# Kernel optimization log

Hardware: AMD Instinct MI355X
Metric: run time of the kernel (lower is better)

The kernel has to match this reference:

```python
import jax, jax.numpy as jnp
import numpy as np

HID, FFN, NE, TOPK = 1024, 4096, 8, 2


def setup_inputs() -> dict:
    key = jax.random.key(0)
    ks = jax.random.split(key, 4)
    x = jax.random.normal(ks[0], (2, 2048, HID), dtype=jnp.float32)
    # router: nn.Linear(hidden, num_experts, bias=False), init std=0.02; stored as [H, E]
    Wr = jax.random.normal(ks[1], (HID, NE), dtype=jnp.float32) * 0.02
    # per-expert FFN weights stacked on leading expert axis
    W1 = jax.random.normal(ks[2], (NE, HID, FFN), dtype=jnp.float32) * (1.0 / np.sqrt(HID))
    b1 = jnp.zeros((NE, FFN), dtype=jnp.float32)
    W2 = jax.random.normal(ks[3], (NE, FFN, HID), dtype=jnp.float32) * (1.0 / np.sqrt(FFN))
    b2 = jnp.zeros((NE, HID), dtype=jnp.float32)
    return {"x": x, "Wr": Wr, "W1": W1, "b1": b1, "W2": W2, "b2": b2}


def reference(x, Wr, W1, b1, W2, b2):
    B, S, H = x.shape
    E = Wr.shape[1]
    T = B * S
    xf = x.reshape(T, H)                                  # [T, H]
    logits = xf @ Wr                                      # [T, E]
    probs = jax.nn.softmax(logits, axis=-1)
    topk_p, topk_i = jax.lax.top_k(probs, TOPK)           # [T, K]
    topk_p = topk_p / jnp.sum(topk_p, axis=-1, keepdims=True)
    # dense combine weights: c[t, e] = normalized prob if expert e selected for token t else 0
    c = jnp.zeros((T, E), dtype=xf.dtype).at[jnp.arange(T)[:, None], topk_i].add(topk_p)

    def expert_step(acc, ew):
        w1, bb1, w2, bb2, ce = ew                         # ce: [T]
        h = jax.nn.gelu(xf @ w1 + bb1, approximate=False)  # exact GELU like nn.GELU()
        y = h @ w2 + bb2                                  # [T, H]
        return acc + ce[:, None] * y, None

    out, _ = jax.lax.scan(expert_step, jnp.zeros_like(xf), (W1, b1, W2, b2, c.T))
    return out.reshape(B, S, H)
```

## Files before the change

kernel.cpp:

```cpp
#include <hip/hip_runtime.h>
#include <hip/hip_bf16.h>

#define H 1024
#define F 4096
#define NE 8
#define T 4096
#define KSPLIT2 2

typedef unsigned short u16;
typedef float floatx4 __attribute__((ext_vector_type(4)));
typedef short short8 __attribute__((ext_vector_type(8)));

__device__ __forceinline__ u16 f2bf(float f) {
  union { float f; unsigned int u; } c; c.f = f;
  unsigned int u = c.u;
  return (u16)((u + 0x7fffu + ((u >> 16) & 1u)) >> 16);
}

__device__ __forceinline__ void load16_lds(const u16* g, u16* l) {
  __builtin_amdgcn_global_load_lds(
      (const __attribute__((address_space(1))) unsigned int*)g,
      (__attribute__((address_space(3))) unsigned int*)l, 16, 0, 0);
}

__global__ __launch_bounds__(256) void router_kernel(
    const float* __restrict__ x, const float* __restrict__ Wr,
    int* __restrict__ cnt, int* __restrict__ tok, float* __restrict__ wgt) {
  int t = (blockIdx.x * 256 + threadIdx.x) >> 6;
  int lane = threadIdx.x & 63;
  const float* xr = x + (size_t)t * H;
  double p[NE];
#pragma unroll
  for (int e = 0; e < NE; ++e) p[e] = 0.0;
  for (int k = lane; k < H; k += 64) {
    float xv = xr[k];
    const float4* wr4 = reinterpret_cast<const float4*>(Wr + k * NE);
    float4 a = wr4[0], b = wr4[1];
    p[0] += (double)xv * a.x; p[1] += (double)xv * a.y;
    p[2] += (double)xv * a.z; p[3] += (double)xv * a.w;
    p[4] += (double)xv * b.x; p[5] += (double)xv * b.y;
    p[6] += (double)xv * b.z; p[7] += (double)xv * b.w;
  }
#pragma unroll
  for (int e = 0; e < NE; ++e) {
#pragma unroll
    for (int off = 32; off; off >>= 1) p[e] += __shfl_down(p[e], off, 64);
  }
  if (lane == 0) {
    int i0 = 0;
#pragma unroll
    for (int e = 1; e < NE; ++e) if (p[e] > p[i0]) i0 = e;
    int i1 = (i0 == 0) ? 1 : 0;
#pragma unroll
    for (int e = 0; e < NE; ++e) if (e != i0 && p[e] > p[i1]) i1 = e;
    double d = exp(p[i1] - p[i0]);
    float w0 = (float)(1.0 / (1.0 + d));
    float w1 = (float)(d / (1.0 + d));
    int pos0 = atomicAdd(&cnt[i0], 1);
    tok[i0 * T + pos0] = t; wgt[i0 * T + pos0] = w0;
    int pos1 = atomicAdd(&cnt[i1], 1);
    tok[i1 * T + pos1] = t; wgt[i1 * T + pos1] = w1;
  }
}

__global__ void offsets_kernel(const int* __restrict__ cnt, int* __restrict__ off) {
  if (threadIdx.x == 0) {
    int s = 0;
#pragma unroll
    for (int e = 0; e < NE; ++e) { off[e] = s; s += cnt[e]; }
    off[NE] = s;
  }
}

__global__ __launch_bounds__(256) void convert_x_kernel(
    const float* __restrict__ x, u16* __restrict__ xb) {
  int i = blockIdx.x * 256 + threadIdx.x;
  float4 v = reinterpret_cast<const float4*>(x)[i];
  ushort4 o;
  o.x = f2bf(v.x); o.y = f2bf(v.y); o.z = f2bf(v.z); o.w = f2bf(v.w);
  reinterpret_cast<ushort4*>(xb)[i] = o;
}

__global__ __launch_bounds__(256) void transpose_bf16_kernel(
    const float* __restrict__ src, u16* __restrict__ dst, int R, int C) {
  __shared__ u16 tile[64][72];
  int e = blockIdx.z;
  int c0 = blockIdx.x << 6, r0 = blockIdx.y << 6;
  const float* s = src + (size_t)e * R * C;
  u16* d = dst + (size_t)e * R * C;
  int t = threadIdx.x;
  int rl = t >> 4, cl = (t & 15) << 2;
#pragma unroll
  for (int i = 0; i < 4; ++i) {
    float4 v = *reinterpret_cast<const float4*>(&s[(size_t)(r0 + rl + i * 16) * C + c0 + cl]);
    ushort4 o; o.x = f2bf(v.x); o.y = f2bf(v.y); o.z = f2bf(v.z); o.w = f2bf(v.w);
    *reinterpret_cast<ushort4*>(&tile[rl + i * 16][cl]) = o;
  }
  __syncthreads();
  int cl2 = t >> 4, rl2 = (t & 15) << 2;
#pragma unroll
  for (int i = 0; i < 4; ++i) {
    ushort4 o;
    o.x = tile[rl2 + 0][cl2 + i * 16];
    o.y = tile[rl2 + 1][cl2 + i * 16];
    o.z = tile[rl2 + 2][cl2 + i * 16];
    o.w = tile[rl2 + 3][cl2 + i * 16];
    *reinterpret_cast<ushort4*>(&d[(size_t)(c0 + cl2 + i * 16) * R + r0 + rl2]) = o;
  }
}

__global__ __launch_bounds__(256) void gemm1_kernel(
    const u16* __restrict__ Xb, const u16* __restrict__ W1t,
    const float* __restrict__ b1, const int* __restrict__ cnt,
    const int* __restrict__ off, const int* __restrict__ tok,
    u16* __restrict__ Hc) {
  int e = blockIdx.z;
  int n = cnt[e];
  int m0 = blockIdx.y << 7;
  if (m0 >= n) return;
  int n0 = blockIdx.x << 7;
  int rb = off[e];

  __shared__ alignas(16) u16 As[128 * 32];
  __shared__ alignas(16) u16 Bs[128 * 32];
  __shared__ int tokS[128];

  int tid = threadIdx.x;
  if (tid < 128) {
    int s = m0 + tid;
    tokS[tid] = (s < n) ? tok[e * T + s] : 0;
  }
  __syncthreads();

  const u16* W1e = W1t + (size_t)e * F * H;
  const u16* aP0 = Xb + (size_t)tokS[tid >> 2] * H + (tid & 3) * 8;
  const u16* aP1 = Xb + (size_t)tokS[64 + (tid >> 2)] * H + (tid & 3) * 8;
  const u16* bP0 = W1e + (size_t)(n0 + (tid >> 2)) * H + (tid & 3) * 8;
  const u16* bP1 = W1e + (size_t)(n0 + 64 + (tid >> 2)) * H + (tid & 3) * 8;
  u16* aL0 = &As[tid * 8];        u16* aL1 = &As[(tid + 256) * 8];
  u16* bL0 = &Bs[tid * 8];        u16* bL1 = &Bs[(tid + 256) * 8];

  int wv = tid >> 6, lane = tid & 63;
  int wm = wv >> 1, wn = wv & 1;
  int quad = lane >> 4, l16 = lane & 15;

  floatx4 acc[4][4];
#pragma unroll
  for (int mt = 0; mt < 4; ++mt)
#pragma unroll
    for (int nt = 0; nt < 4; ++nt) acc[mt][nt] = floatx4{0.f, 0.f, 0.f, 0.f};

  const u16* aF[4]; const u16* bF[4];
#pragma unroll
  for (int i = 0; i < 4; ++i) {
    aF[i] = &As[(wm * 64 + i * 16 + l16) * 32 + quad * 8];
    bF[i] = &Bs[(wn * 64 + i * 16 + l16) * 32 + quad * 8];
  }

  for (int k0 = 0; k0 < H; k0 += 32) {
    load16_lds(aP0 + k0, aL0);
    load16_lds(aP1 + k0, aL1);
    load16_lds(bP0 + k0, bL0);
    load16_lds(bP1 + k0, bL1);
    __syncthreads();
    short8 av[4], bv[4];
#pragma unroll
    for (int i = 0; i < 4; ++i) {
      av[i] = *reinterpret_cast<const short8*>(aF[i]);
      bv[i] = *reinterpret_cast<const short8*>(bF[i]);
    }
#pragma unroll
    for (int mt = 0; mt < 4; ++mt)
#pragma unroll
      for (int nt = 0; nt < 4; ++nt)
        acc[mt][nt] = __builtin_amdgcn_mfma_f32_16x16x32_bf16(av[mt], bv[nt], acc[mt][nt], 0, 0, 0);
    __syncthreads();
  }

  float b1v[4];
#pragma unroll
  for (int nt = 0; nt < 4; ++nt)
    b1v[nt] = b1[e * F + n0 + wn * 64 + nt * 16 + l16];
#pragma unroll
  for (int mt = 0; mt < 4; ++mt) {
#pragma unroll
    for (int i = 0; i < 4; ++i) {
      int row = wm * 64 + mt * 16 + quad * 4 + i;
      int gr = m0 + row;
      if (gr < n) {
        u16* hrow = Hc + (size_t)(rb + gr) * F + n0 + wn * 64 + l16;
#pragma unroll
        for (int nt = 0; nt < 4; ++nt) {
          float v = acc[mt][nt][i] + b1v[nt];
          v = 0.5f * v * (1.0f + erff(v * 0.70710678118f));
          hrow[nt * 16] = f2bf(v);
        }
      }
    }
  }
}

__global__ __launch_bounds__(256) void gemm2_kernel(
    const u16* __restrict__ Hc, const u16* __restrict__ W2t,
    const float* __restrict__ b2, const int* __restrict__ cnt,
    const int* __restrict__ off, const int* __restrict__ tok,
    const float* __restrict__ wgt, float* __restrict__ out) {
  int e = blockIdx.z >> 1;
  int kc = blockIdx.z & 1;
  int n = cnt[e];
  int m0 = blockIdx.y << 7;
  if (m0 >= n) return;
  int n0 = blockIdx.x << 7;
  int rb = off[e];

  __shared__ alignas(16) u16 As[128 * 32];
  __shared__ alignas(16) u16 Bs[128 * 32];

  int tid = threadIdx.x;
  const u16* W2e = W2t + (size_t)e * F * H;
  const u16* aP0 = Hc + (size_t)(rb + m0 + (tid >> 2)) * F + (tid & 3) * 8;
  const u16* aP1 = Hc + (size_t)(rb + m0 + 64 + (tid >> 2)) * F + (tid & 3) * 8;
  const u16* bP0 = W2e + (size_t)(n0 + (tid >> 2)) * F + (tid & 3) * 8;
  const u16* bP1 = W2e + (size_t)(n0 + 64 + (tid >> 2)) * F + (tid & 3) * 8;
  u16* aL0 = &As[tid * 8];        u16* aL1 = &As[(tid + 256) * 8];
  u16* bL0 = &Bs[tid * 8];        u16* bL1 = &Bs[(tid + 256) * 8];

  int wv = tid >> 6, lane = tid & 63;
  int wm = wv >> 1, wn = wv & 1;
  int quad = lane >> 4, l16 = lane & 15;

  floatx4 acc[4][4];
#pragma unroll
  for (int mt = 0; mt < 4; ++mt)
#pragma unroll
    for (int nt = 0; nt < 4; ++nt) acc[mt][nt] = floatx4{0.f, 0.f, 0.f, 0.f};

  const u16* aF[4]; const u16* bF[4];
#pragma unroll
  for (int i = 0; i < 4; ++i) {
    aF[i] = &As[(wm * 64 + i * 16 + l16) * 32 + quad * 8];
    bF[i] = &Bs[(wn * 64 + i * 16 + l16) * 32 + quad * 8];
  }

  const int kBeg = kc * (F / 2);
  const int kEnd = kBeg + (F / 2);
  for (int k0 = kBeg; k0 < kEnd; k0 += 32) {
    load16_lds(aP0 + k0, aL0);
    load16_lds(aP1 + k0, aL1);
    load16_lds(bP0 + k0, bL0);
    load16_lds(bP1 + k0, bL1);
    __syncthreads();
    short8 av[4], bv[4];
#pragma unroll
    for (int i = 0; i < 4; ++i) {
      av[i] = *reinterpret_cast<const short8*>(aF[i]);
      bv[i] = *reinterpret_cast<const short8*>(bF[i]);
    }
#pragma unroll
    for (int mt = 0; mt < 4; ++mt)
#pragma unroll
      for (int nt = 0; nt < 4; ++nt)
        acc[mt][nt] = __builtin_amdgcn_mfma_f32_16x16x32_bf16(av[mt], bv[nt], acc[mt][nt], 0, 0, 0);
    __syncthreads();
  }

  float b2v[4];
#pragma unroll
  for (int nt = 0; nt < 4; ++nt)
    b2v[nt] = (kc == 0) ? b2[e * H + n0 + wn * 64 + nt * 16 + l16] : 0.0f;
#pragma unroll
  for (int mt = 0; mt < 4; ++mt) {
#pragma unroll
    for (int i = 0; i < 4; ++i) {
      int row = wm * 64 + mt * 16 + quad * 4 + i;
      int gr = m0 + row;
      if (gr < n) {
        float wv2 = wgt[e * T + gr];
        int tk = tok[e * T + gr];
        float* orow = out + (size_t)tk * H + n0 + wn * 64 + l16;
#pragma unroll
        for (int nt = 0; nt < 4; ++nt)
          atomicAdd(orow + nt * 16, (acc[mt][nt][i] + b2v[nt]) * wv2);
      }
    }
  }
}

extern "C" void kernel_launch(void* const* d_in, const int* in_sizes, int n_in,
                              void* d_out, int out_size, void* d_ws, size_t ws_size,
                              hipStream_t stream) {
  const float* x  = (const float*)d_in[0];
  const float* Wr = (const float*)d_in[1];
  const float* W1 = (const float*)d_in[2];
  const float* b1 = (const float*)d_in[3];
  const float* W2 = (const float*)d_in[4];
  const float* b2 = (const float*)d_in[5];
  float* out = (float*)d_out;

  char* ws = (char*)d_ws;
  int*   cnt = (int*)(ws + 0);
  int*   off = (int*)(ws + 256);
  int*   tok = (int*)(ws + 4096);
  float* wgt = (float*)(ws + 135168);
  u16*   Xb  = (u16*)(ws + 266240);
  u16*   W1t = (u16*)(ws + 8654848);
  u16*   W2t = (u16*)(ws + 75763712);
  u16*   Hc  = (u16*)(ws + 142872576);

  hipMemsetAsync(cnt, 0, 64, stream);
  hipMemsetAsync(out, 0, (size_t)out_size * sizeof(float), stream);

  router_kernel<<<dim3(T / 4), dim3(256), 0, stream>>>(x, Wr, cnt, tok, wgt);
  offsets_kernel<<<dim3(1), dim3(64), 0, stream>>>(cnt, off);
  convert_x_kernel<<<dim3((T * H / 4) / 256), dim3(256), 0, stream>>>(x, Xb);
  transpose_bf16_kernel<<<dim3(F / 64, H / 64, NE), dim3(256), 0, stream>>>(W1, W1t, H, F);
  transpose_bf16_kernel<<<dim3(H / 64, F / 64, NE), dim3(256), 0, stream>>>(W2, W2t, F, H);
  gemm1_kernel<<<dim3(F / 128, 32, NE), dim3(256), 0, stream>>>(Xb, W1t, b1, cnt, off, tok, Hc);
  gemm2_kernel<<<dim3(H / 128, 32, NE * KSPLIT2), dim3(256), 0, stream>>>(Hc, W2t, b2, cnt, off, tok, wgt, out);
}
```

Baseline: 698.8 us.

## Double-buffer LDS tiles in both expert GEMMs and use a fast GELU approximation

Both expert GEMM kernels now use two LDS buffers, so the global-to-LDS load for the next K tile is issued before the MFMAs on the current tile, removing one barrier per iteration and overlapping memory with compute. The exact erff-based GELU is replaced with the Abramowitz-Stegun polynomial erf approximation, using hardware reciprocal and exp2. Correctness of the double buffering relies on the async LDS loads completing before the single remaining barrier, which the compiler's waitcnt insertion should handle. LDS use per block doubles, which may lower occupancy, and the GELU approximation adds a small error (about 1e-7 absolute).

```diff
diff --git a/kernel.cpp b/kernel.cpp
--- a/kernel.cpp
+++ b/kernel.cpp
@@ -21,6 +21,16 @@
   __builtin_amdgcn_global_load_lds(
       (const __attribute__((address_space(1))) unsigned int*)g,
       (__attribute__((address_space(3))) unsigned int*)l, 16, 0, 0);
+}
+
+__device__ __forceinline__ float gelu_f(float v) {
+  float y = fabsf(v) * 0.70710678118f;
+  float t = __builtin_amdgcn_rcpf(fmaf(0.3275911f, y, 1.0f));
+  float p = t * fmaf(t, fmaf(t, fmaf(t, fmaf(t, 1.061405429f, -1.453152027f),
+                                     1.421413741f), -0.284496736f), 0.254829592f);
+  float e = __builtin_amdgcn_exp2f(-y * y * 1.44269504f);
+  float erfv = fmaf(-p, e, 1.0f);
+  return fmaf(0.5f * fabsf(v), erfv, 0.5f * v);
 }
 
 __global__ __launch_bounds__(256) void router_kernel(
@@ -121,8 +131,8 @@
   int n0 = blockIdx.x << 7;
   int rb = off[e];
 
-  __shared__ alignas(16) u16 As[128 * 32];
-  __shared__ alignas(16) u16 Bs[128 * 32];
+  __shared__ alignas(16) u16 As[2][128 * 32];
+  __shared__ alignas(16) u16 Bs[2][128 * 32];
   __shared__ int tokS[128];
 
   int tid = threadIdx.x;
@@ -137,8 +147,6 @@
   const u16* aP1 = Xb + (size_t)tokS[64 + (tid >> 2)] * H + (tid & 3) * 8;
   const u16* bP0 = W1e + (size_t)(n0 + (tid >> 2)) * H + (tid & 3) * 8;
   const u16* bP1 = W1e + (size_t)(n0 + 64 + (tid >> 2)) * H + (tid & 3) * 8;
-  u16* aL0 = &As[tid * 8];        u16* aL1 = &As[(tid + 256) * 8];
-  u16* bL0 = &Bs[tid * 8];        u16* bL1 = &Bs[(tid + 256) * 8];
 
   int wv = tid >> 6, lane = tid & 63;
   int wm = wv >> 1, wn = wv & 1;
@@ -150,24 +158,31 @@
 #pragma unroll
     for (int nt = 0; nt < 4; ++nt) acc[mt][nt] = floatx4{0.f, 0.f, 0.f, 0.f};
 
-  const u16* aF[4]; const u16* bF[4];
+  int aOff[4], bOff[4];
 #pragma unroll
   for (int i = 0; i < 4; ++i) {
-    aF[i] = &As[(wm * 64 + i * 16 + l16) * 32 + quad * 8];
-    bF[i] = &Bs[(wn * 64 + i * 16 + l16) * 32 + quad * 8];
-  }
-
+    aOff[i] = (wm * 64 + i * 16 + l16) * 32 + quad * 8;
+    bOff[i] = (wn * 64 + i * 16 + l16) * 32 + quad * 8;
+  }
+
+#define STAGE1(buf, kk)                                   \
+  do {                                                    \
+    load16_lds(aP0 + (kk), &As[buf][tid * 8]);            \
+    load16_lds(aP1 + (kk), &As[buf][(tid + 256) * 8]);    \
+    load16_lds(bP0 + (kk), &Bs[buf][tid * 8]);            \
+    load16_lds(bP1 + (kk), &Bs[buf][(tid + 256) * 8]);    \
+  } while (0)
+
+  STAGE1(0, 0);
+  __syncthreads();
+  int cur = 0;
   for (int k0 = 0; k0 < H; k0 += 32) {
-    load16_lds(aP0 + k0, aL0);
-    load16_lds(aP1 + k0, aL1);
-    load16_lds(bP0 + k0, bL0);
-    load16_lds(bP1 + k0, bL1);
-    __syncthreads();
+    if (k0 + 32 < H) STAGE1(cur ^ 1, k0 + 32);
     short8 av[4], bv[4];
 #pragma unroll
     for (int i = 0; i < 4; ++i) {
-      av[i] = *reinterpret_cast<const short8*>(aF[i]);
-      bv[i] = *reinterpret_cast<const short8*>(bF[i]);
+      av[i] = *reinterpret_cast<const short8*>(&As[cur][aOff[i]]);
+      bv[i] = *reinterpret_cast<const short8*>(&Bs[cur][bOff[i]]);
     }
 #pragma unroll
     for (int mt = 0; mt < 4; ++mt)
@@ -175,7 +190,9 @@
       for (int nt = 0; nt < 4; ++nt)
         acc[mt][nt] = __builtin_amdgcn_mfma_f32_16x16x32_bf16(av[mt], bv[nt], acc[mt][nt], 0, 0, 0);
     __syncthreads();
-  }
+    cur ^= 1;
+  }
+#undef STAGE1
 
   float b1v[4];
 #pragma unroll
@@ -192,8 +209,7 @@
 #pragma unroll
         for (int nt = 0; nt < 4; ++nt) {
           float v = acc[mt][nt][i] + b1v[nt];
-          v = 0.5f * v * (1.0f + erff(v * 0.70710678118f));
-          hrow[nt * 16] = f2bf(v);
+          hrow[nt * 16] = f2bf(gelu_f(v));
         }
       }
     }
@@ -213,8 +229,8 @@
   int n0 = blockIdx.x << 7;
   int rb = off[e];
 
-  __shared__ alignas(16) u16 As[128 * 32];
-  __shared__ alignas(16) u16 Bs[128 * 32];
+  __shared__ alignas(16) u16 As[2][128 * 32];
+  __shared__ alignas(16) u16 Bs[2][128 * 32];
 
   int tid = threadIdx.x;
   const u16* W2e = W2t + (size_t)e * F * H;
@@ -222,8 +238,6 @@
   const u16* aP1 = Hc + (size_t)(rb + m0 + 64 + (tid >> 2)) * F + (tid & 3) * 8;
   const u16* bP0 = W2e + (size_t)(n0 + (tid >> 2)) * F + (tid & 3) * 8;
   const u16* bP1 = W2e + (size_t)(n0 + 64 + (tid >> 2)) * F + (tid & 3) * 8;
-  u16* aL0 = &As[tid * 8];        u16* aL1 = &As[(tid + 256) * 8];
-  u16* bL0 = &Bs[tid * 8];        u16* bL1 = &Bs[(tid + 256) * 8];
 
   int wv = tid >> 6, lane = tid & 63;
   int wm = wv >> 1, wn = wv & 1;
@@ -235,26 +249,33 @@
 #pragma unroll
     for (int nt = 0; nt < 4; ++nt) acc[mt][nt] = floatx4{0.f, 0.f, 0.f, 0.f};
 
-  const u16* aF[4]; const u16* bF[4];
+  int aOff[4], bOff[4];
 #pragma unroll
   for (int i = 0; i < 4; ++i) {
-    aF[i] = &As[(wm * 64 + i * 16 + l16) * 32 + quad * 8];
-    bF[i] = &Bs[(wn * 64 + i * 16 + l16) * 32 + quad * 8];
-  }
+    aOff[i] = (wm * 64 + i * 16 + l16) * 32 + quad * 8;
+    bOff[i] = (wn * 64 + i * 16 + l16) * 32 + quad * 8;
+  }
+
+#define STAGE2(buf, kk)                                   \
+  do {                                                    \
+    load16_lds(aP0 + (kk), &As[buf][tid * 8]);            \
+    load16_lds(aP1 + (kk), &As[buf][(tid + 256) * 8]);    \
+    load16_lds(bP0 + (kk), &Bs[buf][tid * 8]);            \
+    load16_lds(bP1 + (kk), &Bs[buf][(tid + 256) * 8]);    \
+  } while (0)
 
   const int kBeg = kc * (F / 2);
   const int kEnd = kBeg + (F / 2);
+  STAGE2(0, kBeg);
+  __syncthreads();
+  int cur = 0;
   for (int k0 = kBeg; k0 < kEnd; k0 += 32) {
-    load16_lds(aP0 + k0, aL0);
-    load16_lds(aP1 + k0, aL1);
-    load16_lds(bP0 + k0, bL0);
-    load16_lds(bP1 + k0, bL1);
-    __syncthreads();
+    if (k0 + 32 < kEnd) STAGE2(cur ^ 1, k0 + 32);
     short8 av[4], bv[4];
 #pragma unroll
     for (int i = 0; i < 4; ++i) {
-      av[i] = *reinterpret_cast<const short8*>(aF[i]);
-      bv[i] = *reinterpret_cast<const short8*>(bF[i]);
+      av[i] = *reinterpret_cast<const short8*>(&As[cur][aOff[i]]);
+      bv[i] = *reinterpret_cast<const short8*>(&Bs[cur][bOff[i]]);
     }
 #pragma unroll
     for (int mt = 0; mt < 4; ++mt)
@@ -262,7 +283,9 @@
       for (int nt = 0; nt < 4; ++nt)
         acc[mt][nt] = __builtin_amdgcn_mfma_f32_16x16x32_bf16(av[mt], bv[nt], acc[mt][nt], 0, 0, 0);
     __syncthreads();
-  }
+    cur ^= 1;
+  }
+#undef STAGE2
 
   float b2v[4];
 #pragma unroll
```

Result: no change. 706.2 us (+1.1%).
